# Kernel tuning notes

Measured on AMD Instinct MI355X. Metric: run time of the kernel, lower is better.

Reference implementation:

```python
import jax, jax.numpy as jnp
import numpy as np

NUM_GROUPS = 2
NUM_VARS = 320
TAU = 2.0  # self.temperature
B, L, CONV_DIM = 8, 4096, 512
CODEVECTOR_DIM = 256


def setup_inputs() -> dict:
    key = jax.random.key(0)
    k1, k2, k3, k4, k5 = jax.random.split(key, 5)
    hidden_states = jax.random.normal(k1, (B, L, CONV_DIM), dtype=jnp.float32)
    gumbel_u = jax.random.uniform(k2, (B * L * NUM_GROUPS, NUM_VARS), dtype=jnp.float32)
    w_proj = jax.random.normal(k3, (CONV_DIM, NUM_GROUPS * NUM_VARS), dtype=jnp.float32) * 0.02
    b_proj = jax.random.normal(k4, (NUM_GROUPS * NUM_VARS,), dtype=jnp.float32) * 0.02
    codevectors = jax.random.normal(k5, (1, NUM_GROUPS * NUM_VARS, CODEVECTOR_DIM // NUM_GROUPS), dtype=jnp.float32)
    return {"hidden_states": hidden_states, "gumbel_u": gumbel_u,
            "w_proj": w_proj, "b_proj": b_proj, "codevectors": codevectors}


def reference(hidden_states, gumbel_u, w_proj, b_proj, codevectors):
    b, l, _ = hidden_states.shape
    G, V = NUM_GROUPS, NUM_VARS
    d = codevectors.shape[-1]

    # weight projection: [B, L, C] @ [C, G*V] -> [B, L, G*V] -> [(B*L*G), V]
    logits = (jnp.einsum('blc,cv->blv', hidden_states, w_proj) + b_proj)
    logits = logits.reshape(b * l * G, V)

    # gumbel-softmax (hard=True, training path) with explicit uniform noise
    eps = 1e-10
    gumbel = -jnp.log(-jnp.log(gumbel_u + eps) + eps)
    y_soft = jax.nn.softmax((logits + gumbel) / TAU, axis=-1)          # [(B*L*G), V]
    idx = jnp.argmax(y_soft, axis=-1)
    y_hard = jax.nn.one_hot(idx, V, dtype=y_soft.dtype)
    # straight-through estimator: hard forward, soft backward
    codevector_probs = y_hard - jax.lax.stop_gradient(y_soft) + y_soft  # [(B*L*G), V]

    # perplexity from the (noise-free) soft distribution, mask=None -> mean over sequences
    soft_dist = jax.nn.softmax(logits.reshape(b * l, G, V), axis=-1)
    avg_probs = jnp.mean(soft_dist, axis=0)                             # [G, V]
    perplexity = jnp.sum(jnp.exp(-jnp.sum(avg_probs * jnp.log(avg_probs + 1e-7), axis=-1)))

    # weighted sum over codevectors per group, then concat groups:
    # probs [(B*L), G, V] x codevectors [G, V, d] -> [(B*L), G, d]
    probs = codevector_probs.reshape(b * l, G, V)
    cv = codevectors.reshape(G, V, d)
    out = jnp.einsum('ngv,gvd->ngd', probs, cv).reshape(b, l, G * d)
    return out, perplexity
```

## Files before the change

### kernel.cpp

```cpp
#include <hip/hip_runtime.h>
#include <math.h>

#define NROWS 32768
#define CDIM  512
#define G_    2
#define V_    320
#define NCOLS 640
#define DCODE 128
#define NSLOT 64
#define BMR   32

typedef short bf16x8 __attribute__((ext_vector_type(8)));
typedef float f32x4  __attribute__((ext_vector_type(4)));

__device__ __forceinline__ short f2bf(float f) {
    union { float f; unsigned u; } v; v.f = f;
    unsigned r = v.u + 0x7FFFu + ((v.u >> 16) & 1u);
    return (short)(r >> 16);
}
__device__ __forceinline__ void gl_lds16(const void* g, void* l) {
    __builtin_amdgcn_global_load_lds(
        (const __attribute__((address_space(1))) unsigned int*)g,
        (__attribute__((address_space(3))) unsigned int*)l, 16, 0, 0);
}

__global__ __launch_bounds__(256) void wprep(const float* __restrict__ w,
                                             short* __restrict__ wpk) {
    int gid = blockIdx.x * 256 + threadIdx.x;
    int l15 = gid & 15, kq = (gid >> 4) & 3;
    int rem = gid >> 6;
    int tt16 = rem % 20; rem /= 20;
    int ts = rem & 15, g = rem >> 4;
    int n  = g * V_ + tt16 * 16 + l15;
    int k0 = ts * 32 + kq * 8;
    bf16x8 o;
    #pragma unroll
    for (int e = 0; e < 8; ++e) o[e] = f2bf(w[(size_t)(k0 + e) * NCOLS + n]);
    *(bf16x8*)&wpk[(size_t)gid * 8] = o;
}

__global__ __launch_bounds__(256) void hprep(const float* __restrict__ hidden,
                                             short* __restrict__ hpk) {
    int gid = blockIdx.x * 256 + threadIdx.x;
    int lane = gid & 63;
    int mf   = (gid >> 6) & 1;
    int ts   = (gid >> 7) & 15;
    int rb   = gid >> 11;
    int row  = rb * BMR + mf * 16 + (lane & 15);
    int k0   = ts * 32 + (lane >> 4) * 8;
    const float* src = hidden + (size_t)row * CDIM + k0;
    float4 a = *(const float4*)src;
    float4 b = *(const float4*)(src + 4);
    bf16x8 o;
    o[0]=f2bf(a.x); o[1]=f2bf(a.y); o[2]=f2bf(a.z); o[3]=f2bf(a.w);
    o[4]=f2bf(b.x); o[5]=f2bf(b.y); o[6]=f2bf(b.z); o[7]=f2bf(b.w);
    *(bf16x8*)&hpk[(size_t)gid * 8] = o;
}

__global__ __launch_bounds__(256, 2) void gvq_gemm(
    const short* __restrict__ hpk,
    const float* __restrict__ gumbel_u,
    const short* __restrict__ wpk,
    const float* __restrict__ bias,
    const float* __restrict__ cv,
    float* __restrict__ out,
    float* __restrict__ gavg)
{
    __shared__ short Hs[16384];
    __shared__ float s_psum[4][BMR];
    __shared__ float s_bestv[4][BMR];
    __shared__ int   s_besti[4][BMR];

    const int t    = threadIdx.x;
    const int wave = t >> 6;
    const int lane = t & 63;
    const int l15  = lane & 15;
    const int kq   = lane >> 4;
    const int tb   = wave * 5;
    const int rb   = blockIdx.x;
    const int g    = blockIdx.y;
    const int m0   = rb * BMR;

    const short* wbase = wpk + ((size_t)(g * 16) * 20 + tb) * 512 + (size_t)lane * 8;

    {
        const short* hsrc = hpk + (size_t)rb * 16384;
        #pragma unroll
        for (int i = 0; i < 8; ++i) {
            const int off = (wave * 8 + i) * 512;
            gl_lds16(hsrc + off + lane * 8, &Hs[off]);
        }
    }

    f32x4 acc[5][2];
    #pragma unroll
    for (int nf = 0; nf < 5; ++nf)
        #pragma unroll
        for (int mf = 0; mf < 2; ++mf)
            #pragma unroll
            for (int r = 0; r < 4; ++r) acc[nf][mf][r] = 0.f;

    bf16x8 bw[5], bn[5];
    #pragma unroll
    for (int nf = 0; nf < 5; ++nf) bw[nf] = *(const bf16x8*)(wbase + nf * 512);
    #pragma unroll
    for (int nf = 0; nf < 5; ++nf) bn[nf] = *(const bf16x8*)(wbase + 10240 + nf * 512);

    __syncthreads();

    #pragma unroll
    for (int ts = 0; ts < 16; ++ts) {
        bf16x8 b2[5];
        if (ts < 14) {
            const short* wn = wbase + (ts + 2) * 10240;
            #pragma unroll
            for (int nf = 0; nf < 5; ++nf) b2[nf] = *(const bf16x8*)(wn + nf * 512);
        }
        bf16x8 hf0 = *(const bf16x8*)&Hs[ts * 1024 + lane * 8];
        bf16x8 hf1 = *(const bf16x8*)&Hs[ts * 1024 + 512 + lane * 8];
        #pragma unroll
        for (int nf = 0; nf < 5; ++nf)
            acc[nf][0] = __builtin_amdgcn_mfma_f32_16x16x32_bf16(bw[nf], hf0, acc[nf][0], 0, 0, 0);
        #pragma unroll
        for (int nf = 0; nf < 5; ++nf)
            acc[nf][1] = __builtin_amdgcn_mfma_f32_16x16x32_bf16(bw[nf], hf1, acc[nf][1], 0, 0, 0);
        #pragma unroll
        for (int nf = 0; nf < 5; ++nf) { bw[nf] = bn[nf]; bn[nf] = b2[nf]; }
    }

    float4 bv4[5], u4[2][5];
    #pragma unroll
    for (int nf = 0; nf < 5; ++nf)
        bv4[nf] = *(const float4*)&bias[g * V_ + (tb + nf) * 16 + kq * 4];
    #pragma unroll
    for (int mf = 0; mf < 2; ++mf) {
        const float* up = gumbel_u + ((size_t)(m0 + mf * 16 + l15) * G_ + g) * V_;
        #pragma unroll
        for (int nf = 0; nf < 5; ++nf)
            u4[mf][nf] = *(const float4*)&up[(tb + nf) * 16 + kq * 4];
    }

    #pragma unroll
    for (int mf = 0; mf < 2; ++mf) {
        float s = 0.f, best = -1e30f; int bi = 0;
        #pragma unroll
        for (int nf = 0; nf < 5; ++nf) {
            #pragma unroll
            for (int r = 0; r < 4; ++r) {
                float z = fminf(acc[nf][mf][r] + bv4[nf][r], 60.f);
                float e = __expf(z);
                acc[nf][mf][r] = e;
                s += e;
                float u = (r == 0) ? u4[mf][nf].x : (r == 1) ? u4[mf][nf].y
                        : (r == 2) ? u4[mf][nf].z : u4[mf][nf].w;
                float wv = -__logf(u + 1e-10f) + 1e-10f;
                float ratio = e * __builtin_amdgcn_rcpf(wv);
                const int vi = (tb + nf) * 16 + kq * 4 + r;
                if (ratio > best) { best = ratio; bi = vi; }
            }
        }
        #pragma unroll
        for (int o = 16; o <= 32; o <<= 1) {
            s += __shfl_xor(s, o);
            float ov = __shfl_xor(best, o);
            int   oi = __shfl_xor(bi, o);
            if (ov > best || (ov == best && oi < bi)) { best = ov; bi = oi; }
        }
        if (kq == 0) {
            s_psum[wave][mf * 16 + l15]  = s;
            s_bestv[wave][mf * 16 + l15] = best;
            s_besti[wave][mf * 16 + l15] = bi;
        }
    }
    __syncthreads();

    float inv[2];
    #pragma unroll
    for (int mf = 0; mf < 2; ++mf) {
        const int rl = mf * 16 + l15;
        inv[mf] = 1.f / (s_psum[0][rl] + s_psum[1][rl] +
                         s_psum[2][rl] + s_psum[3][rl]);
    }
    float cpl[5][4];
    #pragma unroll
    for (int nf = 0; nf < 5; ++nf)
        #pragma unroll
        for (int r = 0; r < 4; ++r) {
            float v = acc[nf][0][r] * inv[0] + acc[nf][1][r] * inv[1];
            #pragma unroll
            for (int o = 1; o <= 8; o <<= 1) v += __shfl_xor(v, o);
            cpl[nf][r] = v;
        }
    float* gslot = gavg + (size_t)(rb & (NSLOT - 1)) * NCOLS;
    if (l15 == 0) {
        #pragma unroll
        for (int nf = 0; nf < 5; ++nf)
            #pragma unroll
            for (int r = 0; r < 4; ++r)
                atomicAdd(&gslot[g * V_ + (tb + nf) * 16 + kq * 4 + r], cpl[nf][r]);
    }

    {
        const int r_  = t >> 3;
        const int seg = t & 7;
        float best = s_bestv[0][r_]; int bi = s_besti[0][r_];
        #pragma unroll
        for (int q = 1; q < 4; ++q) {
            float v = s_bestv[q][r_];
            if (v > best) { best = v; bi = s_besti[q][r_]; }
        }
        const float* src = cv + ((size_t)g * V_ + bi) * DCODE + seg * 16;
        float* dst = out + (size_t)(m0 + r_) * (G_ * DCODE) + g * DCODE + seg * 16;
        #pragma unroll
        for (int j = 0; j < 4; ++j)
            *(float4*)(dst + j * 4) = *(const float4*)(src + j * 4);
    }
}

__global__ __launch_bounds__(1024) void gvq_perp(const float* __restrict__ gavg,
                                                 float* __restrict__ out)
{
    __shared__ float sp[NCOLS];
    const int t = threadIdx.x;
    if (t < NCOLS) {
        float a = 0.f;
        #pragma unroll
        for (int sb = 0; sb < 8; ++sb) {
            float p[8];
            #pragma unroll
            for (int j = 0; j < 8; ++j)
                p[j] = gavg[(size_t)(sb * 8 + j) * NCOLS + t];
            #pragma unroll
            for (int j = 0; j < 8; ++j) a += p[j];
        }
        sp[t] = a;
    }
    __syncthreads();
    if (t < 64) {
        float s0 = 0.f, s1 = 0.f;
        #pragma unroll
        for (int j = 0; j < 5; ++j) {
            float p0 = sp[t + j * 64]      * (1.f / NROWS);
            float p1 = sp[V_ + t + j * 64] * (1.f / NROWS);
            s0 += p0 * __logf(p0 + 1e-7f);
            s1 += p1 * __logf(p1 + 1e-7f);
        }
        #pragma unroll
        for (int o = 1; o < 64; o <<= 1) {
            s0 += __shfl_xor(s0, o);
            s1 += __shfl_xor(s1, o);
        }
        if (t == 0)
            out[(size_t)NROWS * (G_ * DCODE)] = expf(-s0) + expf(-s1);
    }
}

extern "C" void kernel_launch(void* const* d_in, const int* in_sizes, int n_in,
                              void* d_out, int out_size, void* d_ws, size_t ws_size,
                              hipStream_t stream)
{
    const float* hidden = (const float*)d_in[0];
    const float* gu     = (const float*)d_in[1];
    const float* w      = (const float*)d_in[2];
    const float* b      = (const float*)d_in[3];
    const float* cv     = (const float*)d_in[4];
    float* out  = (float*)d_out;
    float* gavg = (float*)d_ws;
    short* wpk  = (short*)((char*)d_ws + 163840);
    short* hpk  = (short*)((char*)d_ws + 819200);

    hipMemsetAsync(d_ws, 0, NSLOT * NCOLS * sizeof(float), stream);
    wprep<<<160, 256, 0, stream>>>(w, wpk);
    hprep<<<8192, 256, 0, stream>>>(hidden, hpk);
    gvq_gemm<<<dim3(NROWS / BMR, G_), 256, 0, stream>>>(hpk, gu, wpk, b, cv, out, gavg);
    gvq_perp<<<1, 1024, 0, stream>>>(gavg, out);
}
```

Before: 86.97 us.

## Double row tile per block to reuse weight fragments across 64 rows

Each GEMM block now processes 64 rows instead of 32 by loading two packed hidden tiles into LDS and running four M-fragments per weight fragment. This halves the number of blocks and the global weight reloads per row, so each weight fragment feeds twice as many MFMAs. The trade-off is double the accumulator registers and LDS per block, which may reduce occupancy below the 2-blocks-per-CU launch bound, and fewer blocks to fill the GPU.

```diff
diff --git a/kernel.cpp b/kernel.cpp
--- a/kernel.cpp
+++ b/kernel.cpp
@@ -8,7 +8,7 @@
 #define NCOLS 640
 #define DCODE 128
 #define NSLOT 64
-#define BMR   32
+#define BMR   64
 
 typedef short bf16x8 __attribute__((ext_vector_type(8)));
 typedef float f32x4  __attribute__((ext_vector_type(4)));
@@ -43,10 +43,10 @@
                                              short* __restrict__ hpk) {
     int gid = blockIdx.x * 256 + threadIdx.x;
     int lane = gid & 63;
-    int mf   = (gid >> 6) & 1;
+    int mfi  = (gid >> 6) & 1;
     int ts   = (gid >> 7) & 15;
     int rb   = gid >> 11;
-    int row  = rb * BMR + mf * 16 + (lane & 15);
+    int row  = rb * 32 + mfi * 16 + (lane & 15);
     int k0   = ts * 32 + (lane >> 4) * 8;
     const float* src = hidden + (size_t)row * CDIM + k0;
     float4 a = *(const float4*)src;
@@ -66,7 +66,7 @@
     float* __restrict__ out,
     float* __restrict__ gavg)
 {
-    __shared__ short Hs[16384];
+    __shared__ short Hs[2][16384];
     __shared__ float s_psum[4][BMR];
     __shared__ float s_bestv[4][BMR];
     __shared__ int   s_besti[4][BMR];
@@ -77,26 +77,27 @@
     const int l15  = lane & 15;
     const int kq   = lane >> 4;
     const int tb   = wave * 5;
-    const int rb   = blockIdx.x;
+    const int bx   = blockIdx.x;
     const int g    = blockIdx.y;
-    const int m0   = rb * BMR;
+    const int m0   = bx * BMR;
 
     const short* wbase = wpk + ((size_t)(g * 16) * 20 + tb) * 512 + (size_t)lane * 8;
 
-    {
-        const short* hsrc = hpk + (size_t)rb * 16384;
+    #pragma unroll
+    for (int h = 0; h < 2; ++h) {
+        const short* hsrc = hpk + (size_t)(bx * 2 + h) * 16384;
         #pragma unroll
         for (int i = 0; i < 8; ++i) {
             const int off = (wave * 8 + i) * 512;
-            gl_lds16(hsrc + off + lane * 8, &Hs[off]);
-        }
-    }
-
-    f32x4 acc[5][2];
+            gl_lds16(hsrc + off + lane * 8, &Hs[h][off]);
+        }
+    }
+
+    f32x4 acc[5][4];
     #pragma unroll
     for (int nf = 0; nf < 5; ++nf)
         #pragma unroll
-        for (int mf = 0; mf < 2; ++mf)
+        for (int mf = 0; mf < 4; ++mf)
             #pragma unroll
             for (int r = 0; r < 4; ++r) acc[nf][mf][r] = 0.f;
 
@@ -116,32 +117,33 @@
             #pragma unroll
             for (int nf = 0; nf < 5; ++nf) b2[nf] = *(const bf16x8*)(wn + nf * 512);
         }
-        bf16x8 hf0 = *(const bf16x8*)&Hs[ts * 1024 + lane * 8];
-        bf16x8 hf1 = *(const bf16x8*)&Hs[ts * 1024 + 512 + lane * 8];
+        bf16x8 hf[4];
+        hf[0] = *(const bf16x8*)&Hs[0][ts * 1024 + lane * 8];
+        hf[1] = *(const bf16x8*)&Hs[0][ts * 1024 + 512 + lane * 8];
+        hf[2] = *(const bf16x8*)&Hs[1][ts * 1024 + lane * 8];
+        hf[3] = *(const bf16x8*)&Hs[1][ts * 1024 + 512 + lane * 8];
         #pragma unroll
         for (int nf = 0; nf < 5; ++nf)
-            acc[nf][0] = __builtin_amdgcn_mfma_f32_16x16x32_bf16(bw[nf], hf0, acc[nf][0], 0, 0, 0);
-        #pragma unroll
-        for (int nf = 0; nf < 5; ++nf)
-            acc[nf][1] = __builtin_amdgcn_mfma_f32_16x16x32_bf16(bw[nf], hf1, acc[nf][1], 0, 0, 0);
+            #pragma unroll
+            for (int mf = 0; mf < 4; ++mf)
+                acc[nf][mf] = __builtin_amdgcn_mfma_f32_16x16x32_bf16(bw[nf], hf[mf], acc[nf][mf], 0, 0, 0);
         #pragma unroll
         for (int nf = 0; nf < 5; ++nf) { bw[nf] = bn[nf]; bn[nf] = b2[nf]; }
     }
 
-    float4 bv4[5], u4[2][5];
+    float4 bv4[5];
     #pragma unroll
     for (int nf = 0; nf < 5; ++nf)
         bv4[nf] = *(const float4*)&bias[g * V_ + (tb + nf) * 16 + kq * 4];
-    #pragma unroll
-    for (int mf = 0; mf < 2; ++mf) {
-        const float* up = gumbel_u + ((size_t)(m0 + mf * 16 + l15) * G_ + g) * V_;
+
+    #pragma unroll
+    for (int mf = 0; mf < 4; ++mf) {
+        const int rl = mf * 16 + l15;
+        const float* up = gumbel_u + ((size_t)(m0 + rl) * G_ + g) * V_;
+        float4 u4[5];
         #pragma unroll
         for (int nf = 0; nf < 5; ++nf)
-            u4[mf][nf] = *(const float4*)&up[(tb + nf) * 16 + kq * 4];
-    }
-
-    #pragma unroll
-    for (int mf = 0; mf < 2; ++mf) {
+            u4[nf] = *(const float4*)&up[(tb + nf) * 16 + kq * 4];
         float s = 0.f, best = -1e30f; int bi = 0;
         #pragma unroll
         for (int nf = 0; nf < 5; ++nf) {
@@ -151,8 +153,8 @@
                 float e = __expf(z);
                 acc[nf][mf][r] = e;
                 s += e;
-                float u = (r == 0) ? u4[mf][nf].x : (r == 1) ? u4[mf][nf].y
-                        : (r == 2) ? u4[mf][nf].z : u4[mf][nf].w;
+                float u = (r == 0) ? u4[nf].x : (r == 1) ? u4[nf].y
+                        : (r == 2) ? u4[nf].z : u4[nf].w;
                 float wv = -__logf(u + 1e-10f) + 1e-10f;
                 float ratio = e * __builtin_amdgcn_rcpf(wv);
                 const int vi = (tb + nf) * 16 + kq * 4 + r;
@@ -167,41 +169,36 @@
             if (ov > best || (ov == best && oi < bi)) { best = ov; bi = oi; }
         }
         if (kq == 0) {
-            s_psum[wave][mf * 16 + l15]  = s;
-            s_bestv[wave][mf * 16 + l15] = best;
-            s_besti[wave][mf * 16 + l15] = bi;
+            s_psum[wave][rl]  = s;
+            s_bestv[wave][rl] = best;
+            s_besti[wave][rl] = bi;
         }
     }
     __syncthreads();
 
-    float inv[2];
-    #pragma unroll
-    for (int mf = 0; mf < 2; ++mf) {
+    float inv[4];
+    #pragma unroll
+    for (int mf = 0; mf < 4; ++mf) {
         const int rl = mf * 16 + l15;
         inv[mf] = 1.f / (s_psum[0][rl] + s_psum[1][rl] +
                          s_psum[2][rl] + s_psum[3][rl]);
     }
-    float cpl[5][4];
     #pragma unroll
     for (int nf = 0; nf < 5; ++nf)
         #pragma unroll
         for (int r = 0; r < 4; ++r) {
-            float v = acc[nf][0][r] * inv[0] + acc[nf][1][r] * inv[1];
+            float v = acc[nf][0][r] * inv[0] + acc[nf][1][r] * inv[1]
+                    + acc[nf][2][r] * inv[2] + acc[nf][3][r] * inv[3];
             #pragma unroll
             for (int o = 1; o <= 8; o <<= 1) v += __shfl_xor(v, o);
-            cpl[nf][r] = v;
-        }
-    float* gslot = gavg + (size_t)(rb & (NSLOT - 1)) * NCOLS;
-    if (l15 == 0) {
-        #pragma unroll
-        for (int nf = 0; nf < 5; ++nf)
-            #pragma unroll
-            for (int r = 0; r < 4; ++r)
-                atomicAdd(&gslot[g * V_ + (tb + nf) * 16 + kq * 4 + r], cpl[nf][r]);
-    }
-
-    {
-        const int r_  = t >> 3;
+            if (l15 == 0)
+                atomicAdd(&gavg[(size_t)(bx & (NSLOT - 1)) * NCOLS
+                                + g * V_ + (tb + nf) * 16 + kq * 4 + r], v);
+        }
+
+    #pragma unroll
+    for (int it = 0; it < 2; ++it) {
+        const int r_  = (t >> 3) + it * 32;
         const int seg = t & 7;
         float best = s_bestv[0][r_]; int bi = s_besti[0][r_];
         #pragma unroll
```

Result: slower. 92.43 us (+6.3%).
